# Kernel optimization log

Hardware: AMD Instinct MI355X
Metric: run time of the kernel (lower is better)

Reference implementation:

```python
import jax, jax.numpy as jnp
import numpy as np


def setup_inputs() -> dict:
    B, S, D, H = 4, 1024, 1024, 16
    key = jax.random.key(0)
    kq, kk, kv, kl, k1, k2, k3, k4 = jax.random.split(key, 8)
    return {
        "queries": jax.random.normal(kq, (B, S, D), dtype=jnp.float32),
        "keys": jax.random.normal(kk, (B, S, D), dtype=jnp.float32),
        "values": jax.random.normal(kv, (B, S, D), dtype=jnp.float32),
        "valid_lens": jax.random.randint(kl, (B,), 1, S + 1, dtype=jnp.int32),
        "Wq": jax.random.normal(k1, (D, D), dtype=jnp.float32) / np.sqrt(D),
        "Wk": jax.random.normal(k2, (D, D), dtype=jnp.float32) / np.sqrt(D),
        "Wv": jax.random.normal(k3, (D, D), dtype=jnp.float32) / np.sqrt(D),
        "Wo": jax.random.normal(k4, (D, D), dtype=jnp.float32) / np.sqrt(D),
        "num_heads": 16,
    }


def reference(queries, keys, values, valid_lens, Wq, Wk, Wv, Wo, num_heads):
    B, Sq, D = queries.shape
    Sk = keys.shape[1]
    H = num_heads
    dh = D // H

    def split_heads(x, W):
        # [B,S,D] @ [D,D] -> [B,H,S,dh]
        return (x @ W).reshape(B, -1, H, dh).transpose(0, 2, 1, 3)

    q = split_heads(queries, Wq)
    k = split_heads(keys, Wk)
    v = split_heads(values, Wv)

    scores = jnp.einsum("bhqd,bhkd->bhqk", q, k) / jnp.sqrt(jnp.float32(dh))
    # masked_softmax: key positions >= valid_len[b] get -1e6 before softmax
    mask = jnp.arange(Sk)[None, None, None, :] < valid_lens[:, None, None, None]
    scores = jnp.where(mask, scores, jnp.float32(-1e6))
    attn = jax.nn.softmax(scores, axis=-1)  # dropout p=0.0 -> identity

    out = jnp.einsum("bhqk,bhkd->bhqd", attn, v)
    out = out.transpose(0, 2, 1, 3).reshape(B, Sq, D)
    return out @ Wo
```

## Files before the change

kernel.cpp:

```cpp
#include <hip/hip_runtime.h>
#include <hip/hip_bf16.h>
#include <cstdint>
#include <cstddef>

typedef __bf16 bf16x8 __attribute__((ext_vector_type(8)));
typedef float  f32x4  __attribute__((ext_vector_type(4)));

__device__ __forceinline__ unsigned short f2bf(float f) {
    unsigned x = __float_as_uint(f);
    return (unsigned short)((x + 0x7fffu + ((x >> 16) & 1u)) >> 16);
}

__device__ __forceinline__ f32x4 mfma16(bf16x8 a, bf16x8 b, f32x4 c) {
    return __builtin_amdgcn_mfma_f32_16x16x32_bf16(a, b, c, 0, 0, 0);
}

__device__ __forceinline__ int swz(int row, int col) {
    return row * 128 + ((((col >> 3) ^ (row & 7)) << 4) | ((col & 7) << 1));
}

template <int BK>
__device__ __forceinline__ int tswz(int row, int col) {
    if constexpr (BK == 64)
        return row * 128 + ((((col >> 3) ^ (row & 7)) << 4) | ((col & 7) << 1));
    else
        return row * 64 + ((((col >> 3) ^ ((row >> 1) & 3)) << 4) | ((col & 7) << 1));
}

#define GLDS16(g, l)                                                          \
    __builtin_amdgcn_global_load_lds(                                         \
        (const __attribute__((address_space(1))) void*)(g),                   \
        (__attribute__((address_space(3))) void*)(l), 16, 0, 0)

__global__ __launch_bounds__(256) void k_cvt(const float4* __restrict__ in,
                                             ushort4* __restrict__ out, int n4) {
    int i = blockIdx.x * 256 + threadIdx.x;
    if (i < n4) {
        float4 v = in[i];
        ushort4 o;
        o.x = f2bf(v.x); o.y = f2bf(v.y); o.z = f2bf(v.z); o.w = f2bf(v.w);
        out[i] = o;
    }
}

__global__ __launch_bounds__(256) void k_cvt_wt(const float* __restrict__ W,
                                                unsigned short* __restrict__ Wt,
                                                int D) {
    __shared__ float tile[32][33];
    int c0 = blockIdx.x * 32, r0 = blockIdx.y * 32;
    int tr = threadIdx.x >> 5, tc = threadIdx.x & 31;
#pragma unroll
    for (int i = 0; i < 4; i++)
        tile[tr + 8 * i][tc] = W[(size_t)(r0 + tr + 8 * i) * D + c0 + tc];
    __syncthreads();
#pragma unroll
    for (int i = 0; i < 4; i++)
        Wt[(size_t)(c0 + tr + 8 * i) * D + r0 + tc] = f2bf(tile[tc][tr + 8 * i]);
}

template <int BK, int TN, typename OutT>
__global__ __launch_bounds__(256) void k_gemm_bt(const unsigned short* __restrict__ A0,
                                                 const unsigned short* __restrict__ Bt0,
                                                 OutT* __restrict__ C0,
                                                 int M, int N, int K,
                                                 size_t aStr, size_t bStr, size_t cStr) {
    constexpr int NF = TN / 32;
    constexpr int SLOTS = BK / 8;
    constexpr int RA = BK / 16;
    constexpr int RB = TN * BK / 2048;

    __shared__ unsigned short As[2][128 * BK];
    __shared__ unsigned short Bs[2][TN * BK];

    const int gxy = gridDim.x * gridDim.y;
    const int nwg = gxy * gridDim.z;
    int wgid = blockIdx.z * gxy + blockIdx.y * gridDim.x + blockIdx.x;
    int sid = (wgid & 7) * (nwg >> 3) + (wgid >> 3);
    const int bz = sid / gxy;
    int rem = sid - bz * gxy;
    const int by = rem / gridDim.x;
    const int bx = rem - by * gridDim.x;

    const unsigned short* A  = A0 + (size_t)bz * aStr;
    const unsigned short* Bt = Bt0 + (size_t)bz * bStr;
    OutT* C = C0 + (size_t)bz * cStr;

    const int t = threadIdx.x;
    const int lane = t & 63, wave = t >> 6;
    const int wr = wave >> 1, wc = wave & 1;
    const int l15 = lane & 15, l4 = lane >> 4;
    const int brow = by * 128, bcol = bx * TN;

    f32x4 zero = {0.f, 0.f, 0.f, 0.f};
    f32x4 acc[4][NF];
#pragma unroll
    for (int m = 0; m < 4; m++)
#pragma unroll
        for (int n = 0; n < NF; n++) acc[m][n] = zero;

    auto stage = [&](int buf, int k0) {
#pragma unroll
        for (int i = 0; i < RA; i++) {
            int c = t + i * 256;
            int row = c / SLOTS;
            int slot = c & (SLOTS - 1);
            int gx = (BK == 64) ? (row & 7) : ((row >> 1) & 3);
            GLDS16(A + (size_t)(brow + row) * K + k0 + (slot ^ gx) * 8,
                   (char*)As[buf] + (size_t)((wave * 64 + i * 256) * 16));
        }
#pragma unroll
        for (int i = 0; i < RB; i++) {
            int c = t + i * 256;
            int row = c / SLOTS;
            int slot = c & (SLOTS - 1);
            int gx = (BK == 64) ? (row & 7) : ((row >> 1) & 3);
            GLDS16(Bt + (size_t)(bcol + row) * K + k0 + (slot ^ gx) * 8,
                   (char*)Bs[buf] + (size_t)((wave * 64 + i * 256) * 16));
        }
    };

    auto compute = [&](int buf) {
#pragma unroll
        for (int ks = 0; ks < BK / 32; ++ks) {
            bf16x8 a[4], b[NF];
#pragma unroll
            for (int m = 0; m < 4; m++) {
                int row = wr * 64 + m * 16 + l15;
                a[m] = *(const bf16x8*)((const char*)As[buf] + tswz<BK>(row, ks * 32 + l4 * 8));
            }
#pragma unroll
            for (int n = 0; n < NF; n++) {
                int row = wc * (TN / 2) + n * 16 + l15;
                b[n] = *(const bf16x8*)((const char*)Bs[buf] + tswz<BK>(row, ks * 32 + l4 * 8));
            }
            __builtin_amdgcn_s_setprio(1);
#pragma unroll
            for (int m = 0; m < 4; m++)
#pragma unroll
                for (int n = 0; n < NF; n++)
                    acc[m][n] = mfma16(a[m], b[n], acc[m][n]);
            __builtin_amdgcn_s_setprio(0);
        }
    };

    const int NT = K / BK;
    stage(0, 0);
    __syncthreads();
    int cur = 0;
    for (int kt = 0; kt < NT - 1; ++kt) {
        stage(cur ^ 1, (kt + 1) * BK);
        compute(cur);
        __syncthreads();
        cur ^= 1;
    }
    compute(cur);

#pragma unroll
    for (int m = 0; m < 4; m++)
#pragma unroll
        for (int n = 0; n < NF; n++)
#pragma unroll
            for (int r = 0; r < 4; r++) {
                int row = brow + wr * 64 + m * 16 + l4 * 4 + r;
                int col = bcol + wc * (TN / 2) + n * 16 + l15;
                float v = acc[m][n][r];
                if constexpr (sizeof(OutT) == 2)
                    ((unsigned short*)C)[(size_t)row * N + col] = f2bf(v);
                else
                    C[(size_t)row * N + col] = v;
            }
}

__global__ __launch_bounds__(256) void k_attn(const unsigned short* __restrict__ Qp,
                                              const unsigned short* __restrict__ Kp,
                                              const unsigned short* __restrict__ Vp,
                                              const int* __restrict__ valid_lens,
                                              unsigned short* __restrict__ AO,
                                              int S, int D) {
    __shared__ unsigned short Ks[2][64 * 64];
    __shared__ unsigned short Vt[2][64 * 64];
    __shared__ unsigned short Ps[64 * 64];

    const int t = threadIdx.x, lane = t & 63, w = t >> 6;
    const int l15 = lane & 15, l4 = lane >> 4;
    const int b = blockIdx.z, h = blockIdx.y, q0 = blockIdx.x * 64;
    const int vl = valid_lens[b];
    const size_t baserow = (size_t)b * S;
    const int hcol = h * 64;
    const int vr = t >> 2, vc0 = (t & 3) * 16;

    bf16x8 aq[2];
#pragma unroll
    for (int ks = 0; ks < 2; ++ks)
        aq[ks] = *(const bf16x8*)&Qp[(baserow + q0 + w * 16 + l15) * D + hcol + ks * 32 + l4 * 8];

    f32x4 zero = {0.f, 0.f, 0.f, 0.f};
    f32x4 oacc[4];
#pragma unroll
    for (int nf = 0; nf < 4; nf++) oacc[nf] = zero;
    float m_run[4], l_run[4];
#pragma unroll
    for (int r = 0; r < 4; r++) { m_run[r] = -1e30f; l_run[r] = 0.f; }

    auto stageK = [&](int buf, int kv0) {
#pragma unroll
        for (int i = 0; i < 2; i++) {
            int c = t + i * 256;
            int row = c >> 3;
            int gcol = ((c & 7) ^ (row & 7)) * 8;
            const unsigned short* gk = Kp + (baserow + kv0 + row) * D + hcol + gcol;
            GLDS16(gk, (char*)Ks[buf] + (size_t)((w * 64 + i * 256) * 16));
        }
    };
    auto loadV = [&](int kv0, bf16x8& v0, bf16x8& v1) {
        const unsigned short* gv = Vp + (baserow + kv0 + vr) * D + hcol + vc0;
        v0 = *(const bf16x8*)gv;
        v1 = *(const bf16x8*)(gv + 8);
    };
    auto writeV = [&](int buf, bf16x8 v0, bf16x8 v1) {
#pragma unroll
        for (int i = 0; i < 8; i++) {
            union { __bf16 h; unsigned short u; } c0, c1;
            c0.h = v0[i]; c1.h = v1[i];
            *(unsigned short*)((char*)Vt[buf] + swz(vc0 + i, vr)) = c0.u;
            *(unsigned short*)((char*)Vt[buf] + swz(vc0 + 8 + i, vr)) = c1.u;
        }
    };

    const int nt = (vl + 63) >> 6;
    stageK(0, 0);
    {
        bf16x8 v0, v1;
        loadV(0, v0, v1);
        writeV(0, v0, v1);
    }

    int cur = 0;
    for (int tt = 0; tt < nt; ++tt) {
        __syncthreads();

        bf16x8 nv0, nv1;
        const bool have_next = (tt + 1) < nt;
        if (have_next) {
            stageK(cur ^ 1, (tt + 1) * 64);
            loadV((tt + 1) * 64, nv0, nv1);
        }

        const int kv0 = tt * 64;
        f32x4 sacc[4];
#pragma unroll
        for (int f = 0; f < 4; f++) {
            sacc[f] = zero;
#pragma unroll
            for (int ks = 0; ks < 2; ++ks) {
                bf16x8 bk = *(const bf16x8*)((const char*)Ks[cur] + swz(f * 16 + l15, ks * 32 + l4 * 8));
                __builtin_amdgcn_s_setprio(1);
                sacc[f] = mfma16(aq[ks], bk, sacc[f]);
                __builtin_amdgcn_s_setprio(0);
            }
        }
#pragma unroll
        for (int f = 0; f < 4; f++) {
            bool masked = (kv0 + f * 16 + l15) >= vl;
#pragma unroll
            for (int r = 0; r < 4; r++) {
                float s = sacc[f][r] * 0.125f;
                sacc[f][r] = masked ? -1e30f : s;
            }
        }
        float mx[4];
#pragma unroll
        for (int r = 0; r < 4; r++)
            mx[r] = fmaxf(fmaxf(sacc[0][r], sacc[1][r]), fmaxf(sacc[2][r], sacc[3][r]));
#pragma unroll
        for (int off = 1; off < 16; off <<= 1)
#pragma unroll
            for (int r = 0; r < 4; r++) mx[r] = fmaxf(mx[r], __shfl_xor(mx[r], off));

        float nm[4], alpha[4], rs[4];
#pragma unroll
        for (int r = 0; r < 4; r++) {
            nm[r] = fmaxf(m_run[r], mx[r]);
            alpha[r] = __expf(m_run[r] - nm[r]);
            m_run[r] = nm[r];
            rs[r] = 0.f;
        }
#pragma unroll
        for (int f = 0; f < 4; f++)
#pragma unroll
            for (int r = 0; r < 4; r++) {
                float p = __expf(sacc[f][r] - nm[r]);
                rs[r] += p;
                *(unsigned short*)((char*)Ps + swz(w * 16 + l4 * 4 + r, f * 16 + l15)) = f2bf(p);
            }
#pragma unroll
        for (int off = 1; off < 16; off <<= 1)
#pragma unroll
            for (int r = 0; r < 4; r++) rs[r] += __shfl_xor(rs[r], off);
#pragma unroll
        for (int r = 0; r < 4; r++) l_run[r] = l_run[r] * alpha[r] + rs[r];
#pragma unroll
        for (int nf = 0; nf < 4; nf++)
#pragma unroll
            for (int r = 0; r < 4; r++) oacc[nf][r] *= alpha[r];

        if (have_next) writeV(cur ^ 1, nv0, nv1);

        asm volatile("s_waitcnt lgkmcnt(0)" ::: "memory");
        __builtin_amdgcn_sched_barrier(0);

        bf16x8 ap[2];
#pragma unroll
        for (int ks = 0; ks < 2; ++ks)
            ap[ks] = *(const bf16x8*)((const char*)Ps + swz(w * 16 + l15, ks * 32 + l4 * 8));
#pragma unroll
        for (int nf = 0; nf < 4; nf++)
#pragma unroll
            for (int ks = 0; ks < 2; ++ks) {
                bf16x8 bv = *(const bf16x8*)((const char*)Vt[cur] + swz(nf * 16 + l15, ks * 32 + l4 * 8));
                __builtin_amdgcn_s_setprio(1);
                oacc[nf] = mfma16(ap[ks], bv, oacc[nf]);
                __builtin_amdgcn_s_setprio(0);
            }
        cur ^= 1;
    }

#pragma unroll
    for (int nf = 0; nf < 4; nf++)
#pragma unroll
        for (int r = 0; r < 4; r++) {
            float v = oacc[nf][r] / l_run[r];
            int row = q0 + w * 16 + l4 * 4 + r;
            AO[(baserow + row) * D + hcol + nf * 16 + l15] = f2bf(v);
        }
}

extern "C" void kernel_launch(void* const* d_in, const int* in_sizes, int n_in,
                              void* d_out, int out_size, void* d_ws, size_t ws_size,
                              hipStream_t stream) {
    const float* q  = (const float*)d_in[0];
    const float* k  = (const float*)d_in[1];
    const float* v  = (const float*)d_in[2];
    const int* vlen = (const int*)d_in[3];
    const float* Wq = (const float*)d_in[4];
    const float* Wk = (const float*)d_in[5];
    const float* Wv = (const float*)d_in[6];
    const float* Wo = (const float*)d_in[7];

    const int B = in_sizes[3];
    const int D = 1024, S = 1024, H = 16;
    const int M = B * S;
    const size_t MB = 1u << 20;

    char* ws = (char*)d_ws;
    unsigned short* X   = (unsigned short*)(ws + 0 * MB);
    unsigned short* Wt  = (unsigned short*)(ws + 24 * MB);
    unsigned short* Wto = (unsigned short*)(ws + 30 * MB);
    unsigned short* P   = (unsigned short*)(ws + 32 * MB);
    unsigned short* Xq  = X;
    unsigned short* Xk  = X + 4 * 1024 * 1024;
    unsigned short* Xv  = X + 8 * 1024 * 1024;
    unsigned short* Wtq = Wt;
    unsigned short* Wtk = Wt + 1024 * 1024;
    unsigned short* Wtv = Wt + 2 * 1024 * 1024;
    unsigned short* Qp  = P;
    unsigned short* Kp  = P + 4 * 1024 * 1024;
    unsigned short* Vp  = P + 8 * 1024 * 1024;
    unsigned short* AO  = Xq;

    int n4 = M * D / 4;
    k_cvt<<<dim3((n4 + 255) / 256), 256, 0, stream>>>((const float4*)q, (ushort4*)Xq, n4);
    k_cvt<<<dim3((n4 + 255) / 256), 256, 0, stream>>>((const float4*)k, (ushort4*)Xk, n4);
    k_cvt<<<dim3((n4 + 255) / 256), 256, 0, stream>>>((const float4*)v, (ushort4*)Xv, n4);
    k_cvt_wt<<<dim3(32, 32), 256, 0, stream>>>(Wq, Wtq, D);
    k_cvt_wt<<<dim3(32, 32), 256, 0, stream>>>(Wk, Wtk, D);
    k_cvt_wt<<<dim3(32, 32), 256, 0, stream>>>(Wv, Wtv, D);
    k_cvt_wt<<<dim3(32, 32), 256, 0, stream>>>(Wo, Wto, D);

    const size_t xStr = (size_t)M * D, wStr = (size_t)D * D;
    k_gemm_bt<32, 128, unsigned short><<<dim3(D / 128, M / 128, 3), 256, 0, stream>>>(
        X, Wt, P, M, D, D, xStr, wStr, xStr);

    k_attn<<<dim3(S / 64, H, B), 256, 0, stream>>>(Qp, Kp, Vp, vlen, AO, S, D);

    k_gemm_bt<32, 64, float><<<dim3(D / 64, M / 128, 1), 256, 0, stream>>>(
        AO, Wto, (float*)d_out, M, D, D, 0, 0, 0);
}
```

Measured before the change: 112.9 us.

## Replace QKV projection GEMM with 256x256-tile 8-wave ping-pong pipelined kernel

Adds a new bf16 GEMM kernel for the fused Q/K/V projection. It uses 256x256 output tiles, 512 threads and BK=64 double-buffered LDS. Global-to-LDS loads for the next tiles are split into eight phases, with barriers and setprio interleaving MFMA work against the loads. The goal is more data reuse per tile and better hiding of memory latency than the previous 128x128 kernel. The cost is fewer workgroups (only 192 across three matrices), which may underfill the GPU, plus heavy register and LDS use.

Measured after the change: 113.7 us. About the same (+0.7%).

```diff
diff --git a/kernel.cpp b/kernel.cpp
--- a/kernel.cpp
+++ b/kernel.cpp
@@ -5,6 +5,8 @@
 
 typedef __bf16 bf16x8 __attribute__((ext_vector_type(8)));
 typedef float  f32x4  __attribute__((ext_vector_type(4)));
+
+template <int V> struct IC { static constexpr int value = V; };
 
 __device__ __forceinline__ unsigned short f2bf(float f) {
     unsigned x = __float_as_uint(f);
@@ -56,6 +58,135 @@
 #pragma unroll
     for (int i = 0; i < 4; i++)
         Wt[(size_t)(c0 + tr + 8 * i) * D + r0 + tc] = f2bf(tile[tc][tr + 8 * i]);
+}
+
+__global__ __launch_bounds__(512, 2) void k_gemm8(const unsigned short* __restrict__ A0,
+                                                  const unsigned short* __restrict__ Bt0,
+                                                  unsigned short* __restrict__ C0,
+                                                  int M, int N, int K,
+                                                  size_t aStr, size_t bStr, size_t cStr) {
+    __shared__ unsigned short As[2][256 * 64];
+    __shared__ unsigned short Bs[2][256 * 64];
+
+    const int gxy = gridDim.x * gridDim.y;
+    const int nwg = gxy * gridDim.z;
+    int wgid = blockIdx.z * gxy + blockIdx.y * gridDim.x + blockIdx.x;
+    int sid = (wgid & 7) * (nwg >> 3) + (wgid >> 3);
+    const int bz = sid / gxy;
+    int rem = sid - bz * gxy;
+    const int by = rem / gridDim.x;
+    const int bx = rem - by * gridDim.x;
+
+    const unsigned short* A  = A0 + (size_t)bz * aStr;
+    const unsigned short* Bt = Bt0 + (size_t)bz * bStr;
+    unsigned short* C = C0 + (size_t)bz * cStr;
+
+    const int t = threadIdx.x, lane = t & 63, w = t >> 6;
+    const int wr = w >> 2, wc = w & 3;
+    const int l15 = lane & 15, l4 = lane >> 4;
+    const int brow = by * 256, bcol = bx * 256;
+
+    f32x4 acc[8][4];
+#pragma unroll
+    for (int m = 0; m < 8; m++)
+#pragma unroll
+        for (int n = 0; n < 4; n++) acc[m][n] = f32x4{0.f, 0.f, 0.f, 0.f};
+
+    auto stA = [&](int buf, int kt, int h) {
+#pragma unroll
+        for (int j = 0; j < 2; j++) {
+            int c = h * 1024 + j * 512 + t;
+            int row = c >> 3, slot = c & 7;
+            GLDS16(A + (size_t)(brow + row) * K + kt * 64 + ((slot ^ (row & 7)) << 3),
+                   (char*)As[buf] + (size_t)(h * 1024 + j * 512 + w * 64) * 16);
+        }
+    };
+    auto stB = [&](int buf, int kt, int h) {
+#pragma unroll
+        for (int j = 0; j < 2; j++) {
+            int c = h * 1024 + j * 512 + t;
+            int row = c >> 3, slot = c & 7;
+            GLDS16(Bt + (size_t)(bcol + row) * K + kt * 64 + ((slot ^ (row & 7)) << 3),
+                   (char*)Bs[buf] + (size_t)(h * 1024 + j * 512 + w * 64) * 16);
+        }
+    };
+
+    bf16x8 b[4][2];
+
+    auto phase = [&](auto BUFC, auto GC, auto RBC, auto stage, auto VMC) {
+        constexpr int BUF = BUFC.value, G = GC.value, VM = VMC.value;
+        constexpr bool RB = RBC.value != 0;
+        bf16x8 a[2][2];
+#pragma unroll
+        for (int i = 0; i < 2; i++)
+#pragma unroll
+            for (int ks = 0; ks < 2; ks++)
+                a[i][ks] = *(const bf16x8*)((const char*)As[BUF] +
+                           swz(wr * 128 + (2 * G + i) * 16 + l15, ks * 32 + l4 * 8));
+        if constexpr (RB) {
+#pragma unroll
+            for (int nf = 0; nf < 4; nf++)
+#pragma unroll
+                for (int ks = 0; ks < 2; ks++)
+                    b[nf][ks] = *(const bf16x8*)((const char*)Bs[BUF] +
+                                swz(wc * 64 + nf * 16 + l15, ks * 32 + l4 * 8));
+        }
+        stage();
+        __builtin_amdgcn_s_barrier();
+        asm volatile("s_waitcnt lgkmcnt(0)" ::: "memory");
+        __builtin_amdgcn_sched_barrier(0);
+        __builtin_amdgcn_s_setprio(1);
+#pragma unroll
+        for (int i = 0; i < 2; i++)
+#pragma unroll
+            for (int nf = 0; nf < 4; nf++)
+#pragma unroll
+                for (int ks = 0; ks < 2; ks++)
+                    acc[2 * G + i][nf] = mfma16(a[i][ks], b[nf][ks], acc[2 * G + i][nf]);
+        __builtin_amdgcn_s_setprio(0);
+        if constexpr (VM == 0) {
+            asm volatile("s_waitcnt vmcnt(0)" ::: "memory");
+            __builtin_amdgcn_sched_barrier(0);
+        } else if constexpr (VM > 0) {
+            asm volatile("s_waitcnt vmcnt(4)" ::: "memory");
+            __builtin_amdgcn_sched_barrier(0);
+        }
+        __builtin_amdgcn_s_barrier();
+    };
+
+    auto iter = [&](int t0, auto LASTC) {
+        constexpr bool LAST = LASTC.value != 0;
+        phase(IC<0>{}, IC<0>{}, IC<1>{}, [&] { stA(1, t0 + 1, 0); }, IC<-1>{});
+        phase(IC<0>{}, IC<1>{}, IC<0>{}, [&] { stA(1, t0 + 1, 1); }, IC<-1>{});
+        phase(IC<0>{}, IC<2>{}, IC<0>{}, [&] { if constexpr (!LAST) stB(0, t0 + 2, 0); }, IC<-1>{});
+        phase(IC<0>{}, IC<3>{}, IC<0>{}, [&] { if constexpr (!LAST) stB(0, t0 + 2, 1); },
+              IC<LAST ? 0 : 4>{});
+        phase(IC<1>{}, IC<0>{}, IC<1>{}, [&] { if constexpr (!LAST) stA(0, t0 + 2, 0); }, IC<-1>{});
+        phase(IC<1>{}, IC<1>{}, IC<0>{}, [&] { if constexpr (!LAST) stA(0, t0 + 2, 1); }, IC<-1>{});
+        phase(IC<1>{}, IC<2>{}, IC<0>{}, [&] { if constexpr (!LAST) stB(1, t0 + 3, 0); }, IC<-1>{});
+        phase(IC<1>{}, IC<3>{}, IC<0>{}, [&] { if constexpr (!LAST) stB(1, t0 + 3, 1); },
+              IC<LAST ? -1 : 4>{});
+    };
+
+    stA(0, 0, 0); stA(0, 0, 1);
+    stB(0, 0, 0); stB(0, 0, 1);
+    stB(1, 1, 0); stB(1, 1, 1);
+    __syncthreads();
+
+    const int NIT = K >> 7;
+    for (int it = 0; it < NIT - 1; ++it) iter(2 * it, IC<0>{});
+    iter(2 * (NIT - 1), IC<1>{});
+
+#pragma unroll
+    for (int mf = 0; mf < 8; mf++)
+#pragma unroll
+        for (int nf = 0; nf < 4; nf++)
+#pragma unroll
+            for (int r = 0; r < 4; r++) {
+                int row = brow + wr * 128 + mf * 16 + l4 * 4 + r;
+                int col = bcol + wc * 64 + nf * 16 + l15;
+                C[(size_t)row * N + col] = f2bf(acc[mf][nf][r]);
+            }
 }
 
 template <int BK, int TN, typename OutT>
@@ -378,7 +509,7 @@
     k_cvt_wt<<<dim3(32, 32), 256, 0, stream>>>(Wo, Wto, D);
 
     const size_t xStr = (size_t)M * D, wStr = (size_t)D * D;
-    k_gemm_bt<32, 128, unsigned short><<<dim3(D / 128, M / 128, 3), 256, 0, stream>>>(
+    k_gemm8<<<dim3(D / 256, M / 256, 3), 512, 0, stream>>>(
         X, Wt, P, M, D, D, xStr, wStr, xStr);
 
     k_attn<<<dim3(S / 64, H, B), 256, 0, stream>>>(Qp, Kp, Vp, vlen, AO, S, D);
```

## Fuse fp32-to-bf16 activation conversion into QKV GEMM and batch weight conversions

Applied to the files above, without the earlier changes.

Removes the three standalone activation conversion kernels by loading fp32 Q/K/V inputs directly in the QKV projection GEMM and converting to bf16 in registers before writing swizzled LDS. The four weight transpose-conversions are merged into one launch using blockIdx.z. The output projection GEMM's K tile grows from 32 to 64. This avoids writing and re-reading 24MB of bf16 activations plus launch overhead, but the GEMM now reads fp32 A (twice the bytes per tile) through registers instead of direct-to-LDS loads, which may stall the pipeline.

After: 99.70 us. 1.13x faster.

```diff
diff --git a/kernel.cpp b/kernel.cpp
--- a/kernel.cpp
+++ b/kernel.cpp
@@ -32,21 +32,16 @@
         (const __attribute__((address_space(1))) void*)(g),                   \
         (__attribute__((address_space(3))) void*)(l), 16, 0, 0)
 
-__global__ __launch_bounds__(256) void k_cvt(const float4* __restrict__ in,
-                                             ushort4* __restrict__ out, int n4) {
-    int i = blockIdx.x * 256 + threadIdx.x;
-    if (i < n4) {
-        float4 v = in[i];
-        ushort4 o;
-        o.x = f2bf(v.x); o.y = f2bf(v.y); o.z = f2bf(v.z); o.w = f2bf(v.w);
-        out[i] = o;
-    }
-}
-
-__global__ __launch_bounds__(256) void k_cvt_wt(const float* __restrict__ W,
-                                                unsigned short* __restrict__ Wt,
-                                                int D) {
+__global__ __launch_bounds__(256) void k_cvt_wt4(const float* __restrict__ W0,
+                                                 const float* __restrict__ W1,
+                                                 const float* __restrict__ W2,
+                                                 const float* __restrict__ W3,
+                                                 unsigned short* __restrict__ out,
+                                                 int D) {
     __shared__ float tile[32][33];
+    const float* W = (blockIdx.z == 0) ? W0 : (blockIdx.z == 1) ? W1
+                    : (blockIdx.z == 2) ? W2 : W3;
+    unsigned short* Wt = out + (size_t)blockIdx.z * D * D;
     int c0 = blockIdx.x * 32, r0 = blockIdx.y * 32;
     int tr = threadIdx.x >> 5, tc = threadIdx.x & 31;
 #pragma unroll
@@ -56,6 +51,130 @@
 #pragma unroll
     for (int i = 0; i < 4; i++)
         Wt[(size_t)(c0 + tr + 8 * i) * D + r0 + tc] = f2bf(tile[tc][tr + 8 * i]);
+}
+
+__global__ __launch_bounds__(256) void k_gemm_qkv(const float* __restrict__ Xq,
+                                                  const float* __restrict__ Xk,
+                                                  const float* __restrict__ Xv,
+                                                  const unsigned short* __restrict__ Wt0,
+                                                  unsigned short* __restrict__ P0,
+                                                  int M, int N, int K) {
+    constexpr int BK = 32, TN = 128;
+    constexpr int NF = TN / 32;
+    constexpr int SLOTS = BK / 8;
+    constexpr int RB = TN * BK / 2048;
+
+    __shared__ unsigned short As[2][128 * BK];
+    __shared__ unsigned short Bs[2][TN * BK];
+
+    const int gxy = gridDim.x * gridDim.y;
+    const int nwg = gxy * gridDim.z;
+    int wgid = blockIdx.z * gxy + blockIdx.y * gridDim.x + blockIdx.x;
+    int sid = (wgid & 7) * (nwg >> 3) + (wgid >> 3);
+    const int bz = sid / gxy;
+    int rem = sid - bz * gxy;
+    const int by = rem / gridDim.x;
+    const int bx = rem - by * gridDim.x;
+
+    const float* Af = (bz == 0) ? Xq : (bz == 1) ? Xk : Xv;
+    const unsigned short* Bt = Wt0 + (size_t)bz * (size_t)K * N;
+    unsigned short* C = P0 + (size_t)bz * (size_t)M * N;
+
+    const int t = threadIdx.x;
+    const int lane = t & 63, wave = t >> 6;
+    const int wr = wave >> 1, wc = wave & 1;
+    const int l15 = lane & 15, l4 = lane >> 4;
+    const int brow = by * 128, bcol = bx * TN;
+
+    const int arow = t >> 1, ach = (t & 1) * 16;
+    float4 va[4];
+
+    auto loadA = [&](int k0) {
+        const float* ga = Af + (size_t)(brow + arow) * K + k0 + ach;
+#pragma unroll
+        for (int j = 0; j < 4; j++) va[j] = *(const float4*)(ga + 4 * j);
+    };
+    auto writeA = [&](int buf) {
+        union { unsigned short u[8]; uint4 v; } o0, o1;
+#pragma unroll
+        for (int j = 0; j < 2; j++) {
+            o0.u[4 * j + 0] = f2bf(va[j].x);
+            o0.u[4 * j + 1] = f2bf(va[j].y);
+            o0.u[4 * j + 2] = f2bf(va[j].z);
+            o0.u[4 * j + 3] = f2bf(va[j].w);
+            o1.u[4 * j + 0] = f2bf(va[j + 2].x);
+            o1.u[4 * j + 1] = f2bf(va[j + 2].y);
+            o1.u[4 * j + 2] = f2bf(va[j + 2].z);
+            o1.u[4 * j + 3] = f2bf(va[j + 2].w);
+        }
+        *(uint4*)((char*)As[buf] + tswz<BK>(arow, ach)) = o0.v;
+        *(uint4*)((char*)As[buf] + tswz<BK>(arow, ach + 8)) = o1.v;
+    };
+    auto stageB = [&](int buf, int k0) {
+#pragma unroll
+        for (int i = 0; i < RB; i++) {
+            int c = t + i * 256;
+            int row = c / SLOTS;
+            int slot = c & (SLOTS - 1);
+            GLDS16(Bt + (size_t)(bcol + row) * K + k0 + ((slot ^ ((row >> 1) & 3)) << 3),
+                   (char*)Bs[buf] + (size_t)((wave * 64 + i * 256) * 16));
+        }
+    };
+
+    f32x4 zero = {0.f, 0.f, 0.f, 0.f};
+    f32x4 acc[4][NF];
+#pragma unroll
+    for (int m = 0; m < 4; m++)
+#pragma unroll
+        for (int n = 0; n < NF; n++) acc[m][n] = zero;
+
+    auto compute = [&](int buf) {
+        bf16x8 a[4], b[NF];
+#pragma unroll
+        for (int m = 0; m < 4; m++) {
+            int row = wr * 64 + m * 16 + l15;
+            a[m] = *(const bf16x8*)((const char*)As[buf] + tswz<BK>(row, l4 * 8));
+        }
+#pragma unroll
+        for (int n = 0; n < NF; n++) {
+            int row = wc * (TN / 2) + n * 16 + l15;
+            b[n] = *(const bf16x8*)((const char*)Bs[buf] + tswz<BK>(row, l4 * 8));
+        }
+        __builtin_amdgcn_s_setprio(1);
+#pragma unroll
+        for (int m = 0; m < 4; m++)
+#pragma unroll
+            for (int n = 0; n < NF; n++)
+                acc[m][n] = mfma16(a[m], b[n], acc[m][n]);
+        __builtin_amdgcn_s_setprio(0);
+    };
+
+    const int NT = K / BK;
+    loadA(0);
+    writeA(0);
+    stageB(0, 0);
+    __syncthreads();
+    int cur = 0;
+    for (int kt = 0; kt < NT - 1; ++kt) {
+        loadA((kt + 1) * BK);
+        stageB(cur ^ 1, (kt + 1) * BK);
+        compute(cur);
+        writeA(cur ^ 1);
+        __syncthreads();
+        cur ^= 1;
+    }
+    compute(cur);
+
+#pragma unroll
+    for (int m = 0; m < 4; m++)
+#pragma unroll
+        for (int n = 0; n < NF; n++)
+#pragma unroll
+            for (int r = 0; r < 4; r++) {
+                int row = brow + wr * 64 + m * 16 + l4 * 4 + r;
+                int col = bcol + wc * (TN / 2) + n * 16 + l15;
+                C[(size_t)row * N + col] = f2bf(acc[m][n][r]);
+            }
 }
 
 template <int BK, int TN, typename OutT>
@@ -353,36 +472,21 @@
     const size_t MB = 1u << 20;
 
     char* ws = (char*)d_ws;
-    unsigned short* X   = (unsigned short*)(ws + 0 * MB);
+    unsigned short* AO  = (unsigned short*)(ws + 0 * MB);
     unsigned short* Wt  = (unsigned short*)(ws + 24 * MB);
     unsigned short* Wto = (unsigned short*)(ws + 30 * MB);
     unsigned short* P   = (unsigned short*)(ws + 32 * MB);
-    unsigned short* Xq  = X;
-    unsigned short* Xk  = X + 4 * 1024 * 1024;
-    unsigned short* Xv  = X + 8 * 1024 * 1024;
-    unsigned short* Wtq = Wt;
-    unsigned short* Wtk = Wt + 1024 * 1024;
-    unsigned short* Wtv = Wt + 2 * 1024 * 1024;
     unsigned short* Qp  = P;
     unsigned short* Kp  = P + 4 * 1024 * 1024;
     unsigned short* Vp  = P + 8 * 1024 * 1024;
-    unsigned short* AO  = Xq;
-
-    int n4 = M * D / 4;
-    k_cvt<<<dim3((n4 + 255) / 256), 256, 0, stream>>>((const float4*)q, (ushort4*)Xq, n4);
-    k_cvt<<<dim3((n4 + 255) / 256), 256, 0, stream>>>((const float4*)k, (ushort4*)Xk, n4);
-    k_cvt<<<dim3((n4 + 255) / 256), 256, 0, stream>>>((const float4*)v, (ushort4*)Xv, n4);
-    k_cvt_wt<<<dim3(32, 32), 256, 0, stream>>>(Wq, Wtq, D);
-    k_cvt_wt<<<dim3(32, 32), 256, 0, stream>>>(Wk, Wtk, D);
-    k_cvt_wt<<<dim3(32, 32), 256, 0, stream>>>(Wv, Wtv, D);
-    k_cvt_wt<<<dim3(32, 32), 256, 0, stream>>>(Wo, Wto, D);
-
-    const size_t xStr = (size_t)M * D, wStr = (size_t)D * D;
-    k_gemm_bt<32, 128, unsigned short><<<dim3(D / 128, M / 128, 3), 256, 0, stream>>>(
-        X, Wt, P, M, D, D, xStr, wStr, xStr);
+
+    k_cvt_wt4<<<dim3(32, 32, 4), 256, 0, stream>>>(Wq, Wk, Wv, Wo, Wt, D);
+
+    k_gemm_qkv<<<dim3(D / 128, M / 128, 3), 256, 0, stream>>>(
+        q, k, v, Wt, P, M, D, D);
 
     k_attn<<<dim3(S / 64, H, B), 256, 0, stream>>>(Qp, Kp, Vp, vlen, AO, S, D);
 
-    k_gemm_bt<32, 64, float><<<dim3(D / 64, M / 128, 1), 256, 0, stream>>>(
+    k_gemm_bt<64, 64, float><<<dim3(D / 64, M / 128, 1), 256, 0, stream>>>(
         AO, Wto, (float*)d_out, M, D, D, 0, 0, 0);
 }
```

## Fuse prep conversions and skip K/V rows beyond valid length

Applied to the files above, without the earlier changes.

Merges the three activation conversions and four weight transposes into one prep kernel, saving launch overhead. In both the conversion and the Q/K/V projection GEMM, it skips K and V rows whose sequence position is at or beyond valid_lens[b], since the mask zeroes their attention weight. The GEMMs also move to 64x64 tiles with BK=64, which gives more blocks to spread the early exits over. This relies on the attention kernel never reading the skipped K/V rows; if it does read them, the uninitialised values are multiplied by zero weights, and NaN or Inf garbage could leak through.

Result: faster. 98.65 us (-12.6%).

```diff
diff --git a/kernel.cpp b/kernel.cpp
--- a/kernel.cpp
+++ b/kernel.cpp
@@ -32,44 +32,61 @@
         (const __attribute__((address_space(1))) void*)(g),                   \
         (__attribute__((address_space(3))) void*)(l), 16, 0, 0)
 
-__global__ __launch_bounds__(256) void k_cvt(const float4* __restrict__ in,
-                                             ushort4* __restrict__ out, int n4) {
-    int i = blockIdx.x * 256 + threadIdx.x;
-    if (i < n4) {
+__global__ __launch_bounds__(256) void k_prep(const float4* __restrict__ i0,
+                                              const float4* __restrict__ i1,
+                                              const float4* __restrict__ i2,
+                                              ushort4* __restrict__ xout,
+                                              const float* __restrict__ W0,
+                                              const float* __restrict__ W1,
+                                              const float* __restrict__ W2,
+                                              const float* __restrict__ W3,
+                                              unsigned short* __restrict__ wout,
+                                              int D, const int* __restrict__ vlen) {
+    __shared__ float tile[32][33];
+    const int bid = blockIdx.x;
+    if (bid < 12288) {
+        int z = bid >> 12, rowb = bid & 4095;
+        if (z) {
+            if ((rowb & 1023) >= vlen[rowb >> 10]) return;
+        }
+        const float4* in = (z == 0) ? i0 : (z == 1) ? i1 : i2;
+        int i = rowb * 256 + threadIdx.x;
         float4 v = in[i];
         ushort4 o;
         o.x = f2bf(v.x); o.y = f2bf(v.y); o.z = f2bf(v.z); o.w = f2bf(v.w);
-        out[i] = o;
+        xout[(size_t)z * 1048576 + i] = o;
+    } else {
+        int wid = bid - 12288;
+        int z = wid >> 10, t2 = wid & 1023;
+        int bx = t2 & 31, by = t2 >> 5;
+        const float* W = (z == 0) ? W0 : (z == 1) ? W1 : (z == 2) ? W2 : W3;
+        unsigned short* Wt = wout + (size_t)z * D * D;
+        int c0 = bx * 32, r0 = by * 32;
+        int tr = threadIdx.x >> 5, tc = threadIdx.x & 31;
+#pragma unroll
+        for (int i = 0; i < 4; i++)
+            tile[tr + 8 * i][tc] = W[(size_t)(r0 + tr + 8 * i) * D + c0 + tc];
+        __syncthreads();
+#pragma unroll
+        for (int i = 0; i < 4; i++)
+            Wt[(size_t)(c0 + tr + 8 * i) * D + r0 + tc] = f2bf(tile[tc][tr + 8 * i]);
     }
 }
 
-__global__ __launch_bounds__(256) void k_cvt_wt(const float* __restrict__ W,
-                                                unsigned short* __restrict__ Wt,
-                                                int D) {
-    __shared__ float tile[32][33];
-    int c0 = blockIdx.x * 32, r0 = blockIdx.y * 32;
-    int tr = threadIdx.x >> 5, tc = threadIdx.x & 31;
-#pragma unroll
-    for (int i = 0; i < 4; i++)
-        tile[tr + 8 * i][tc] = W[(size_t)(r0 + tr + 8 * i) * D + c0 + tc];
-    __syncthreads();
-#pragma unroll
-    for (int i = 0; i < 4; i++)
-        Wt[(size_t)(c0 + tr + 8 * i) * D + r0 + tc] = f2bf(tile[tc][tr + 8 * i]);
-}
-
-template <int BK, int TN, typename OutT>
+template <int BK, int TM, int TN, typename OutT>
 __global__ __launch_bounds__(256) void k_gemm_bt(const unsigned short* __restrict__ A0,
                                                  const unsigned short* __restrict__ Bt0,
                                                  OutT* __restrict__ C0,
                                                  int M, int N, int K,
-                                                 size_t aStr, size_t bStr, size_t cStr) {
+                                                 size_t aStr, size_t bStr, size_t cStr,
+                                                 const int* __restrict__ vlen) {
+    constexpr int NM = TM / 32;
     constexpr int NF = TN / 32;
     constexpr int SLOTS = BK / 8;
-    constexpr int RA = BK / 16;
+    constexpr int RA = TM * BK / 2048;
     constexpr int RB = TN * BK / 2048;
 
-    __shared__ unsigned short As[2][128 * BK];
+    __shared__ unsigned short As[2][TM * BK];
     __shared__ unsigned short Bs[2][TN * BK];
 
     const int gxy = gridDim.x * gridDim.y;
@@ -81,6 +98,12 @@
     const int by = rem / gridDim.x;
     const int bx = rem - by * gridDim.x;
 
+    if (vlen && bz >= 1) {
+        int srow = (by * TM) & 1023;
+        int bb = (by * TM) >> 10;
+        if (srow >= vlen[bb]) return;
+    }
+
     const unsigned short* A  = A0 + (size_t)bz * aStr;
     const unsigned short* Bt = Bt0 + (size_t)bz * bStr;
     OutT* C = C0 + (size_t)bz * cStr;
@@ -89,12 +112,12 @@
     const int lane = t & 63, wave = t >> 6;
     const int wr = wave >> 1, wc = wave & 1;
     const int l15 = lane & 15, l4 = lane >> 4;
-    const int brow = by * 128, bcol = bx * TN;
+    const int brow = by * TM, bcol = bx * TN;
 
     f32x4 zero = {0.f, 0.f, 0.f, 0.f};
-    f32x4 acc[4][NF];
-#pragma unroll
-    for (int m = 0; m < 4; m++)
+    f32x4 acc[NM][NF];
+#pragma unroll
+    for (int m = 0; m < NM; m++)
 #pragma unroll
         for (int n = 0; n < NF; n++) acc[m][n] = zero;
 
@@ -122,10 +145,10 @@
     auto compute = [&](int buf) {
 #pragma unroll
         for (int ks = 0; ks < BK / 32; ++ks) {
-            bf16x8 a[4], b[NF];
-#pragma unroll
-            for (int m = 0; m < 4; m++) {
-                int row = wr * 64 + m * 16 + l15;
+            bf16x8 a[NM], b[NF];
+#pragma unroll
+            for (int m = 0; m < NM; m++) {
+                int row = wr * (TM / 2) + m * 16 + l15;
                 a[m] = *(const bf16x8*)((const char*)As[buf] + tswz<BK>(row, ks * 32 + l4 * 8));
             }
 #pragma unroll
@@ -135,7 +158,7 @@
             }
             __builtin_amdgcn_s_setprio(1);
 #pragma unroll
-            for (int m = 0; m < 4; m++)
+            for (int m = 0; m < NM; m++)
 #pragma unroll
                 for (int n = 0; n < NF; n++)
                     acc[m][n] = mfma16(a[m], b[n], acc[m][n]);
@@ -156,12 +179,12 @@
     compute(cur);
 
 #pragma unroll
-    for (int m = 0; m < 4; m++)
+    for (int m = 0; m < NM; m++)
 #pragma unroll
         for (int n = 0; n < NF; n++)
 #pragma unroll
             for (int r = 0; r < 4; r++) {
-                int row = brow + wr * 64 + m * 16 + l4 * 4 + r;
+                int row = brow + wr * (TM / 2) + m * 16 + l4 * 4 + r;
                 int col = bcol + wc * (TN / 2) + n * 16 + l15;
                 float v = acc[m][n][r];
                 if constexpr (sizeof(OutT) == 2)
@@ -357,32 +380,21 @@
     unsigned short* Wt  = (unsigned short*)(ws + 24 * MB);
     unsigned short* Wto = (unsigned short*)(ws + 30 * MB);
     unsigned short* P   = (unsigned short*)(ws + 32 * MB);
-    unsigned short* Xq  = X;
-    unsigned short* Xk  = X + 4 * 1024 * 1024;
-    unsigned short* Xv  = X + 8 * 1024 * 1024;
-    unsigned short* Wtq = Wt;
-    unsigned short* Wtk = Wt + 1024 * 1024;
-    unsigned short* Wtv = Wt + 2 * 1024 * 1024;
     unsigned short* Qp  = P;
     unsigned short* Kp  = P + 4 * 1024 * 1024;
     unsigned short* Vp  = P + 8 * 1024 * 1024;
-    unsigned short* AO  = Xq;
-
-    int n4 = M * D / 4;
-    k_cvt<<<dim3((n4 + 255) / 256), 256, 0, stream>>>((const float4*)q, (ushort4*)Xq, n4);
-    k_cvt<<<dim3((n4 + 255) / 256), 256, 0, stream>>>((const float4*)k, (ushort4*)Xk, n4);
-    k_cvt<<<dim3((n4 + 255) / 256), 256, 0, stream>>>((const float4*)v, (ushort4*)Xv, n4);
-    k_cvt_wt<<<dim3(32, 32), 256, 0, stream>>>(Wq, Wtq, D);
-    k_cvt_wt<<<dim3(32, 32), 256, 0, stream>>>(Wk, Wtk, D);
-    k_cvt_wt<<<dim3(32, 32), 256, 0, stream>>>(Wv, Wtv, D);
-    k_cvt_wt<<<dim3(32, 32), 256, 0, stream>>>(Wo, Wto, D);
+    unsigned short* AO  = X;
+
+    k_prep<<<dim3(16384), 256, 0, stream>>>(
+        (const float4*)q, (const float4*)k, (const float4*)v, (ushort4*)X,
+        Wq, Wk, Wv, Wo, Wt, D, vlen);
 
     const size_t xStr = (size_t)M * D, wStr = (size_t)D * D;
-    k_gemm_bt<32, 128, unsigned short><<<dim3(D / 128, M / 128, 3), 256, 0, stream>>>(
-        X, Wt, P, M, D, D, xStr, wStr, xStr);
+    k_gemm_bt<64, 64, 64, unsigned short><<<dim3(D / 64, M / 64, 3), 256, 0, stream>>>(
+        X, Wt, P, M, D, D, xStr, wStr, xStr, vlen);
 
     k_attn<<<dim3(S / 64, H, B), 256, 0, stream>>>(Qp, Kp, Vp, vlen, AO, S, D);
 
-    k_gemm_bt<32, 64, float><<<dim3(D / 64, M / 128, 1), 256, 0, stream>>>(
-        AO, Wto, (float*)d_out, M, D, D, 0, 0, 0);
-}
+    k_gemm_bt<64, 64, 64, float><<<dim3(D / 64, M / 64, 1), 256, 0, stream>>>(
+        AO, Wto, (float*)d_out, M, D, D, 0, 0, 0, nullptr);
+}
```
